# Kernel tuning notes

Hardware: AMD Instinct MI355X
Metric: run time of the kernel (lower is better)

The kernel has to match this reference:

```python
import jax, jax.numpy as jnp
import numpy as np
import math

D_MODEL = 1024
NUM_HEADS = 16
HEAD_DIM = D_MODEL // NUM_HEADS
WINDOW = 5  # positions j with i - W//2 <= j <= i + W//2 are visible


def setup_inputs() -> dict:
    key = jax.random.key(0)
    ks = jax.random.split(key, 9)
    B, S = 2, 2048
    x = jax.random.normal(ks[0], (B, S, D_MODEL), dtype=jnp.float32)
    # Xavier-uniform linear weights [out, in] (torch convention), zero biases
    lim = math.sqrt(6.0 / (D_MODEL + D_MODEL))
    def w(k):
        return jax.random.uniform(k, (D_MODEL, D_MODEL), dtype=jnp.float32, minval=-lim, maxval=lim)
    return {
        'x': x,
        'Wq': w(ks[1]), 'bq': jnp.zeros((D_MODEL,), jnp.float32),
        'Wk': w(ks[2]), 'bk': jnp.zeros((D_MODEL,), jnp.float32),
        'Wv': w(ks[3]), 'bv': jnp.zeros((D_MODEL,), jnp.float32),
        'Wo': w(ks[4]), 'bo': jnp.zeros((D_MODEL,), jnp.float32),
    }


def reference(x, Wq, bq, Wk, bk, Wv, bv, Wo, bo):
    B, S, D = x.shape
    H, hd = NUM_HEADS, HEAD_DIM
    half = WINDOW // 2

    def proj(W, b):
        # torch Linear: y = x @ W.T + b ; split heads -> [B, H, S, hd]
        return (jnp.einsum('bsd,ed->bse', x, W) + b).reshape(B, S, H, hd).transpose(0, 2, 1, 3)

    q = proj(Wq, bq)
    k = proj(Wk, bk)
    v = proj(Wv, bv)

    scores = jnp.einsum('bhqd,bhkd->bhqk', q, k) / jnp.sqrt(jnp.asarray(hd, x.dtype))
    i = jnp.arange(S)[:, None]
    j = jnp.arange(S)[None, :]
    band = (j >= i - half) & (j <= i + half)  # [S, S] local window mask
    scores = jnp.where(band, scores, jnp.asarray(-1e9, x.dtype))
    attn = jax.nn.softmax(scores, axis=-1)  # dropout is identity in eval mode
    out = jnp.einsum('bhqk,bhkd->bhqd', attn, v)
    out = out.transpose(0, 2, 1, 3).reshape(B, S, D)
    return jnp.einsum('bsd,ed->bse', out, Wo) + bo
```

## Files before the change

### kernel.cpp

```cpp
#include <hip/hip_runtime.h>
#include <hip/hip_bf16.h>

typedef __bf16 bf16_t;
typedef __bf16 bf16x4 __attribute__((ext_vector_type(4)));
typedef __bf16 bf16x8 __attribute__((ext_vector_type(8)));
typedef float f32x4 __attribute__((ext_vector_type(4)));

#define S_LEN 2048
#define DMODEL 1024
#define NHEADS 16
#define HDIM 64
#define BROWS 4096
#define QKVN 3072

__device__ __forceinline__ void async16(const void* g, void* l) {
  __builtin_amdgcn_global_load_lds(
      (const __attribute__((address_space(1))) void*)g,
      (__attribute__((address_space(3))) void*)l, 16, 0, 0);
}

__global__ __launch_bounds__(256) void cvt_all_kernel(
    const float* __restrict__ x, const float* __restrict__ Wq,
    const float* __restrict__ Wk, const float* __restrict__ Wv,
    const float* __restrict__ Wo, bf16_t* __restrict__ dst) {
  const int i = blockIdx.x * 256 + threadIdx.x;
  constexpr int XN4 = (BROWS * DMODEL) / 4;
  constexpr int WN4 = (DMODEL * DMODEL) / 4;
  const float* src;
  size_t off;
  if (i < XN4) {
    src = x;
    off = (size_t)i;
  } else {
    const int wi = i - XN4;
    const int w = wi >> 18;
    off = (size_t)(wi & (WN4 - 1));
    src = (w == 0) ? Wq : (w == 1) ? Wk : (w == 2) ? Wv : Wo;
  }
  const float4 v = *(const float4*)(src + off * 4);
  bf16x4 o;
  o[0] = (bf16_t)v.x;
  o[1] = (bf16_t)v.y;
  o[2] = (bf16_t)v.z;
  o[3] = (bf16_t)v.w;
  *(bf16x4*)(dst + (size_t)i * 4) = o;
}

#define BARR __builtin_amdgcn_s_barrier()
#define LGKM0 asm volatile("s_waitcnt lgkmcnt(0)" ::: "memory")
#define VMC3 asm volatile("s_waitcnt vmcnt(3)" ::: "memory")
#define VMC0 asm volatile("s_waitcnt vmcnt(0)" ::: "memory")

__global__ __launch_bounds__(512, 2) void gemm_qkv256_kernel(
    const bf16_t* __restrict__ A, const bf16_t* __restrict__ W,
    const float* __restrict__ bq, const float* __restrict__ bk,
    const float* __restrict__ bv, bf16_t* __restrict__ C) {
  constexpr int Kd = 1024;
  __shared__ char lds[114688];
  char* ldsA = lds;
  char* ldsB = lds + 65536;

  const int m0 = blockIdx.x * 256;
  const int n0 = blockIdx.y * 192;

  const int tid = threadIdx.x;
  const int lane = tid & 63;
  const int wid = tid >> 6;
  const int wr = wid >> 2;
  const int wc = wid & 3;
  const int fr = lane & 15;
  const int l16 = lane >> 4;

  f32x4 acc[8][3] = {};
  bf16x8 aA[4][2], bB[3][2];

  auto stageA = [&](int buf, int h, int kt) {
#pragma unroll
    for (int l = 0; l < 2; ++l) {
      const int idx = l * 512 + tid;
      const int r = idx >> 3;
      const int slot = idx & 7;
      async16((const char*)(A + (size_t)(m0 + h * 128 + r) * Kd + kt * 64 +
                            ((slot ^ (r & 7)) << 3)),
              ldsA + buf * 32768 + h * 16384 + r * 128 + slot * 16);
    }
  };
  auto stageB = [&](int buf, int th, int kt) {
    const int r = tid >> 3;
    const int slot = tid & 7;
    async16((const char*)(W + (size_t)(n0 + th * 64 + r) * Kd + kt * 64 +
                          ((slot ^ (r & 7)) << 3)),
            ldsB + buf * 24576 + th * 8192 + r * 128 + slot * 16);
  };

  auto rdA = [&](int buf, int row, int ks) -> bf16x8 {
    return *(const bf16x8*)(ldsA + buf * 32768 + row * 128 +
                            ((((ks << 2) + l16) ^ (row & 7)) << 4));
  };
  auto rdB = [&](int buf, int row, int ks) -> bf16x8 {
    return *(const bf16x8*)(ldsB + buf * 24576 + row * 128 +
                            ((((ks << 2) + l16) ^ (row & 7)) << 4));
  };

#define RDA(MH, BUF)                                                     \
  _Pragma("unroll") for (int m_ = 0; m_ < 4; ++m_)                       \
      _Pragma("unroll") for (int ks_ = 0; ks_ < 2; ++ks_) aA[m_][ks_] =  \
          rdA(BUF, wr * 128 + (MH)*64 + m_ * 16 + fr, ks_);
#define RDB(NF0, NC, BUF)                                                \
  _Pragma("unroll") for (int n_ = 0; n_ < (NC); ++n_)                    \
      _Pragma("unroll") for (int ks_ = 0; ks_ < 2; ++ks_)                \
          bB[(NF0) + n_][ks_] =                                          \
              rdB(BUF, wc * 48 + ((NF0) + n_) * 16 + fr, ks_);
#define MMAQ(MH, NF0, NC)                                                     \
  _Pragma("unroll") for (int m_ = 0; m_ < 4; ++m_)                            \
      _Pragma("unroll") for (int n_ = 0; n_ < (NC); ++n_) {                   \
    acc[(MH)*4 + m_][(NF0) + n_] = __builtin_amdgcn_mfma_f32_16x16x32_bf16(   \
        aA[m_][0], bB[(NF0) + n_][0], acc[(MH)*4 + m_][(NF0) + n_], 0, 0, 0); \
    acc[(MH)*4 + m_][(NF0) + n_] = __builtin_amdgcn_mfma_f32_16x16x32_bf16(   \
        aA[m_][1], bB[(NF0) + n_][1], acc[(MH)*4 + m_][(NF0) + n_], 0, 0, 0); \
  }

  stageA(0, 0, 0);
  stageA(0, 1, 0);
  stageB(0, 0, 0);
  stageB(0, 1, 0);
  stageB(0, 2, 0);
  stageB(1, 0, 1);
  stageB(1, 1, 1);
  stageB(1, 2, 1);
  VMC3;
  BARR;

#pragma unroll 1
  for (int i = 0; i < 8; ++i) {
    const int t0 = 2 * i, t1 = 2 * i + 1;
    const bool st = (i < 7);
    RDA(0, 0);
    RDB(0, 2, 0);
    stageA(1, 0, t1);
    BARR;
    LGKM0;
    __builtin_amdgcn_s_setprio(1);
    MMAQ(0, 0, 2);
    __builtin_amdgcn_s_setprio(0);
    BARR;
    RDB(2, 1, 0);
    stageA(1, 1, t1);
    BARR;
    LGKM0;
    __builtin_amdgcn_s_setprio(1);
    MMAQ(0, 2, 1);
    __builtin_amdgcn_s_setprio(0);
    BARR;
    RDA(1, 0);
    if (st) stageB(0, 0, t0 + 2);
    BARR;
    LGKM0;
    __builtin_amdgcn_s_setprio(1);
    MMAQ(1, 0, 2);
    __builtin_amdgcn_s_setprio(0);
    BARR;
    if (st) {
      stageB(0, 1, t0 + 2);
      stageB(0, 2, t0 + 2);
    }
    __builtin_amdgcn_s_setprio(1);
    MMAQ(1, 2, 1);
    __builtin_amdgcn_s_setprio(0);
    if (st) {
      VMC3;
    } else {
      VMC0;
    }
    BARR;
    RDA(0, 1);
    RDB(0, 2, 1);
    if (st) stageA(0, 0, t0 + 2);
    BARR;
    LGKM0;
    __builtin_amdgcn_s_setprio(1);
    MMAQ(0, 0, 2);
    __builtin_amdgcn_s_setprio(0);
    BARR;
    RDB(2, 1, 1);
    if (st) stageA(0, 1, t0 + 2);
    BARR;
    LGKM0;
    __builtin_amdgcn_s_setprio(1);
    MMAQ(0, 2, 1);
    __builtin_amdgcn_s_setprio(0);
    BARR;
    RDA(1, 1);
    if (st) stageB(1, 0, t1 + 2);
    BARR;
    LGKM0;
    __builtin_amdgcn_s_setprio(1);
    MMAQ(1, 0, 2);
    __builtin_amdgcn_s_setprio(0);
    BARR;
    if (st) {
      stageB(1, 1, t1 + 2);
      stageB(1, 2, t1 + 2);
    }
    __builtin_amdgcn_s_setprio(1);
    MMAQ(1, 2, 1);
    __builtin_amdgcn_s_setprio(0);
    if (st) VMC3;
    BARR;
  }
#undef RDA
#undef RDB
#undef MMAQ

  const int cr = l16 * 4;
#pragma unroll
  for (int nf = 0; nf < 3; ++nf) {
    const int col = n0 + wc * 48 + nf * 16 + fr;
    const int mat = col >> 10;
    const float* bp = (mat == 0) ? bq : (mat == 1) ? bk : bv;
    const float bval = bp[col & 1023];
#pragma unroll
    for (int mf = 0; mf < 8; ++mf) {
      const int row = m0 + wr * 128 + mf * 16 + cr;
#pragma unroll
      for (int r = 0; r < 4; ++r)
        C[(size_t)(row + r) * QKVN + col] = (bf16_t)(acc[mf][nf][r] + bval);
    }
  }
}

template <typename OutT>
__device__ __forceinline__ void gemm_body(
    const bf16_t* __restrict__ A, const bf16_t* __restrict__ W,
    const float* __restrict__ bias, OutT* __restrict__ C, int m0, int n0) {
  constexpr int Kd = 1024, Nd = 1024, BK = 32, NT = Kd / BK;
  __shared__ bf16_t ldsA[2][128 * BK];
  __shared__ bf16_t ldsB[2][128 * BK];

  const int tid = threadIdx.x;
  const int lane = tid & 63;
  const int wave = tid >> 6;
  const int wr = wave >> 1;
  const int wc = wave & 1;

  f32x4 acc[4][4] = {};

  const int fr = lane & 15;
  const int ko = (lane >> 4) * 8;

  auto stage = [&](int buf, int t) {
    const int k0 = t * BK;
#pragma unroll
    for (int p = 0; p < 2; ++p) {
      const int off = (p * 256 + tid) * 16;
      const int row = off >> 6;
      const int kb = off & 63;
      async16((const char*)(A + (size_t)(m0 + row) * Kd + k0) + kb,
              (char*)ldsA[buf] + off);
      async16((const char*)(W + (size_t)(n0 + row) * Kd + k0) + kb,
              (char*)ldsB[buf] + off);
    }
  };

  auto compute = [&](int buf) {
    bf16x8 af[4], bfr[4];
#pragma unroll
    for (int i = 0; i < 4; ++i)
      af[i] = *(const bf16x8*)(ldsA[buf] + (wr * 64 + i * 16 + fr) * BK + ko);
#pragma unroll
    for (int j = 0; j < 4; ++j)
      bfr[j] = *(const bf16x8*)(ldsB[buf] + (wc * 64 + j * 16 + fr) * BK + ko);
#pragma unroll
    for (int i = 0; i < 4; ++i)
#pragma unroll
      for (int j = 0; j < 4; ++j)
        acc[i][j] = __builtin_amdgcn_mfma_f32_16x16x32_bf16(af[i], bfr[j],
                                                            acc[i][j], 0, 0, 0);
  };

  stage(0, 0);
  __syncthreads();
#pragma unroll 1
  for (int t = 0; t < NT; ++t) {
    if (t + 1 < NT) stage((t + 1) & 1, t + 1);
    compute(t & 1);
    __syncthreads();
  }

  const int cr = (lane >> 4) * 4;
#pragma unroll
  for (int j = 0; j < 4; ++j) {
    const int col = n0 + wc * 64 + j * 16 + fr;
    const float bval = bias[col];
#pragma unroll
    for (int i = 0; i < 4; ++i) {
#pragma unroll
      for (int r = 0; r < 4; ++r) {
        const int row = m0 + wr * 64 + i * 16 + cr + r;
        C[(size_t)row * Nd + col] = (OutT)(acc[i][j][r] + bval);
      }
    }
  }
}

__global__ __launch_bounds__(256) void gemm_o_kernel(
    const bf16_t* __restrict__ ctx, const bf16_t* __restrict__ Wob,
    const float* __restrict__ bo, float* __restrict__ out) {
  gemm_body<float>(ctx, Wob, bo, out, blockIdx.x * 128, blockIdx.y * 128);
}

#define CHUNK 256
#define TROWS 260

__global__ __launch_bounds__(256) void attn_kernel(
    const bf16_t* __restrict__ QKV, bf16_t* __restrict__ ctx) {
  __shared__ bf16_t ldsK[TROWS * HDIM];
  __shared__ bf16_t ldsV[TROWS * HDIM];

  const int tid = threadIdx.x;
  const int blk = blockIdx.x;
  const int chunk = blk & 7;
  const int bh = blk >> 3;
  const int h = bh & (NHEADS - 1);
  const int b = bh >> 4;
  const int s0 = chunk * CHUNK;

  const bf16_t* Kb = QKV + (size_t)b * S_LEN * QKVN + DMODEL + h * HDIM;
  const bf16_t* Vb = QKV + (size_t)b * S_LEN * QKVN + 2 * DMODEL + h * HDIM;

#pragma unroll
  for (int j = 0; j < 9; ++j) {
    const int i = j * 256 + tid;
    if (i < TROWS * 8) {
      const int tr = i >> 3;
      const int slot = i & 7;
      const int c = slot ^ (tr & 7);
      int gs = s0 - 2 + tr;
      gs = (gs < 0) ? 0 : (gs >= S_LEN ? S_LEN - 1 : gs);
      async16((const char*)(Kb + (size_t)gs * QKVN) + c * 16,
              (char*)ldsK + i * 16);
      async16((const char*)(Vb + (size_t)gs * QKVN) + c * 16,
              (char*)ldsV + i * 16);
    }
  }

  const int s = s0 + tid;
  const bf16_t* Qrow = QKV + ((size_t)(b * S_LEN) + s) * QKVN + h * HDIM;
  bf16x8 q8[8];
#pragma unroll
  for (int c = 0; c < 8; ++c) q8[c] = *(const bf16x8*)(Qrow + c * 8);
  float qf[64];
#pragma unroll
  for (int c = 0; c < 8; ++c)
#pragma unroll
    for (int e = 0; e < 8; ++e) qf[c * 8 + e] = (float)q8[c][e];

  __syncthreads();

  float sc[5];
#pragma unroll
  for (int jj = 0; jj < 5; ++jj) {
    const int tr = tid + jj;
    float d = 0.f;
#pragma unroll
    for (int c = 0; c < 8; ++c) {
      const bf16x8 k8 = *(const bf16x8*)(ldsK + tr * HDIM + (c ^ (tr & 7)) * 8);
#pragma unroll
      for (int e = 0; e < 8; ++e) d += qf[c * 8 + e] * (float)k8[e];
    }
    const int j = s - 2 + jj;
    sc[jj] = (j < 0 || j >= S_LEN) ? -1e30f : d * 0.125f;
  }

  float m = sc[0];
#pragma unroll
  for (int jj = 1; jj < 5; ++jj) m = fmaxf(m, sc[jj]);
  float p[5], l = 0.f;
#pragma unroll
  for (int jj = 0; jj < 5; ++jj) {
    p[jj] = __expf(sc[jj] - m);
    l += p[jj];
  }
  const float inv = 1.0f / l;
#pragma unroll
  for (int jj = 0; jj < 5; ++jj) p[jj] *= inv;

  float o[64];
#pragma unroll
  for (int e = 0; e < 64; ++e) o[e] = 0.f;
#pragma unroll
  for (int jj = 0; jj < 5; ++jj) {
    const int tr = tid + jj;
    const float pj = p[jj];
#pragma unroll
    for (int c = 0; c < 8; ++c) {
      const bf16x8 v8 = *(const bf16x8*)(ldsV + tr * HDIM + (c ^ (tr & 7)) * 8);
#pragma unroll
      for (int e = 0; e < 8; ++e) o[c * 8 + e] += pj * (float)v8[e];
    }
  }

  bf16_t* Crow = (bf16_t*)ctx + ((size_t)(b * S_LEN) + s) * DMODEL + h * HDIM;
#pragma unroll
  for (int c = 0; c < 8; ++c) {
    bf16x8 ov;
#pragma unroll
    for (int e = 0; e < 8; ++e) ov[e] = (bf16_t)o[c * 8 + e];
    *(bf16x8*)(Crow + c * 8) = ov;
  }
}

extern "C" void kernel_launch(void* const* d_in, const int* in_sizes, int n_in,
                              void* d_out, int out_size, void* d_ws,
                              size_t ws_size, hipStream_t stream) {
  const float* x = (const float*)d_in[0];
  const float* Wq = (const float*)d_in[1];
  const float* bq = (const float*)d_in[2];
  const float* Wk = (const float*)d_in[3];
  const float* bk = (const float*)d_in[4];
  const float* Wv = (const float*)d_in[5];
  const float* bv = (const float*)d_in[6];
  const float* Wo = (const float*)d_in[7];
  const float* bo = (const float*)d_in[8];
  float* out = (float*)d_out;

  const size_t mat = (size_t)BROWS * DMODEL;
  const size_t wmat = (size_t)DMODEL * DMODEL;
  bf16_t* xb = (bf16_t*)d_ws;
  bf16_t* Wqkv = xb + mat;
  bf16_t* Wob = Wqkv + 3 * wmat;
  bf16_t* QKV = Wob + wmat;
  bf16_t* ctx = QKV + 3 * mat;

  cvt_all_kernel<<<8192, 256, 0, stream>>>(x, Wq, Wk, Wv, Wo, xb);

  gemm_qkv256_kernel<<<dim3(16, 16), 512, 0, stream>>>(xb, Wqkv, bq, bk, bv,
                                                       QKV);
  attn_kernel<<<256, 256, 0, stream>>>(QKV, ctx);
  gemm_o_kernel<<<dim3(32, 8), 256, 0, stream>>>(ctx, Wob, bo, out);
}
```

Measured before the change: 80.07 us.

## Double-buffer A fragments in registers and drop explicit LDS waits in QKV GEMM

The QKV GEMM main loop now keeps two register sets for A fragments. Both halves are read from LDS ahead of use, and the next k-tile's first half is prefetched before the closing barrier. The explicit lgkmcnt(0) waits are removed and replaced with sched_barrier fences, leaving the compiler to insert waits. The aim is to cut the number of LDS-read/barrier/MFMA phases and overlap LDS reads with MFMA work, at the cost of more VGPRs under a 512-thread, 2-block launch bound, which risks spills or lower occupancy.

```diff
diff --git a/kernel.cpp b/kernel.cpp
--- a/kernel.cpp
+++ b/kernel.cpp
@@ -47,7 +47,7 @@
 }
 
 #define BARR __builtin_amdgcn_s_barrier()
-#define LGKM0 asm volatile("s_waitcnt lgkmcnt(0)" ::: "memory")
+#define SB0 __builtin_amdgcn_sched_barrier(0)
 #define VMC3 asm volatile("s_waitcnt vmcnt(3)" ::: "memory")
 #define VMC0 asm volatile("s_waitcnt vmcnt(0)" ::: "memory")
 
@@ -72,7 +72,7 @@
   const int l16 = lane >> 4;
 
   f32x4 acc[8][3] = {};
-  bf16x8 aA[4][2], bB[3][2];
+  bf16x8 aS0[4][2], aS1[4][2], bB[3][2];
 
   auto stageA = [&](int buf, int h, int kt) {
 #pragma unroll
@@ -102,22 +102,22 @@
                             ((((ks << 2) + l16) ^ (row & 7)) << 4));
   };
 
-#define RDA(MH, BUF)                                                     \
+#define RDA_TO(AS, MH, BUF)                                              \
   _Pragma("unroll") for (int m_ = 0; m_ < 4; ++m_)                       \
-      _Pragma("unroll") for (int ks_ = 0; ks_ < 2; ++ks_) aA[m_][ks_] =  \
+      _Pragma("unroll") for (int ks_ = 0; ks_ < 2; ++ks_) AS[m_][ks_] =  \
           rdA(BUF, wr * 128 + (MH)*64 + m_ * 16 + fr, ks_);
 #define RDB(NF0, NC, BUF)                                                \
   _Pragma("unroll") for (int n_ = 0; n_ < (NC); ++n_)                    \
       _Pragma("unroll") for (int ks_ = 0; ks_ < 2; ++ks_)                \
           bB[(NF0) + n_][ks_] =                                          \
               rdB(BUF, wc * 48 + ((NF0) + n_) * 16 + fr, ks_);
-#define MMAQ(MH, NF0, NC)                                                     \
+#define MMAQ(AS, MH, NF0, NC)                                                 \
   _Pragma("unroll") for (int m_ = 0; m_ < 4; ++m_)                            \
       _Pragma("unroll") for (int n_ = 0; n_ < (NC); ++n_) {                   \
     acc[(MH)*4 + m_][(NF0) + n_] = __builtin_amdgcn_mfma_f32_16x16x32_bf16(   \
-        aA[m_][0], bB[(NF0) + n_][0], acc[(MH)*4 + m_][(NF0) + n_], 0, 0, 0); \
+        AS[m_][0], bB[(NF0) + n_][0], acc[(MH)*4 + m_][(NF0) + n_], 0, 0, 0); \
     acc[(MH)*4 + m_][(NF0) + n_] = __builtin_amdgcn_mfma_f32_16x16x32_bf16(   \
-        aA[m_][1], bB[(NF0) + n_][1], acc[(MH)*4 + m_][(NF0) + n_], 0, 0, 0); \
+        AS[m_][1], bB[(NF0) + n_][1], acc[(MH)*4 + m_][(NF0) + n_], 0, 0, 0); \
   }
 
   stageA(0, 0, 0);
@@ -130,85 +130,94 @@
   stageB(1, 2, 1);
   VMC3;
   BARR;
+  RDA_TO(aS0, 0, 0);
 
 #pragma unroll 1
   for (int i = 0; i < 8; ++i) {
     const int t0 = 2 * i, t1 = 2 * i + 1;
     const bool st = (i < 7);
-    RDA(0, 0);
     RDB(0, 2, 0);
+    RDA_TO(aS1, 1, 0);
     stageA(1, 0, t1);
-    BARR;
-    LGKM0;
-    __builtin_amdgcn_s_setprio(1);
-    MMAQ(0, 0, 2);
+    SB0;
+    BARR;
+    __builtin_amdgcn_s_setprio(1);
+    MMAQ(aS0, 0, 0, 2);
     __builtin_amdgcn_s_setprio(0);
     BARR;
     RDB(2, 1, 0);
     stageA(1, 1, t1);
-    BARR;
-    LGKM0;
-    __builtin_amdgcn_s_setprio(1);
-    MMAQ(0, 2, 1);
-    __builtin_amdgcn_s_setprio(0);
-    BARR;
-    RDA(1, 0);
+    SB0;
+    BARR;
+    __builtin_amdgcn_s_setprio(1);
+    MMAQ(aS0, 0, 2, 1);
+    __builtin_amdgcn_s_setprio(0);
+    BARR;
     if (st) stageB(0, 0, t0 + 2);
-    BARR;
-    LGKM0;
-    __builtin_amdgcn_s_setprio(1);
-    MMAQ(1, 0, 2);
+    SB0;
+    BARR;
+    __builtin_amdgcn_s_setprio(1);
+    MMAQ(aS1, 1, 0, 2);
     __builtin_amdgcn_s_setprio(0);
     BARR;
     if (st) {
       stageB(0, 1, t0 + 2);
       stageB(0, 2, t0 + 2);
     }
-    __builtin_amdgcn_s_setprio(1);
-    MMAQ(1, 2, 1);
-    __builtin_amdgcn_s_setprio(0);
+    SB0;
+    __builtin_amdgcn_s_setprio(1);
+    MMAQ(aS1, 1, 2, 1);
+    __builtin_amdgcn_s_setprio(0);
+    SB0;
     if (st) {
       VMC3;
     } else {
       VMC0;
     }
-    BARR;
-    RDA(0, 1);
+    RDA_TO(aS0, 0, 1);
+    SB0;
+    BARR;
     RDB(0, 2, 1);
+    RDA_TO(aS1, 1, 1);
     if (st) stageA(0, 0, t0 + 2);
-    BARR;
-    LGKM0;
-    __builtin_amdgcn_s_setprio(1);
-    MMAQ(0, 0, 2);
+    SB0;
+    BARR;
+    __builtin_amdgcn_s_setprio(1);
+    MMAQ(aS0, 0, 0, 2);
     __builtin_amdgcn_s_setprio(0);
     BARR;
     RDB(2, 1, 1);
     if (st) stageA(0, 1, t0 + 2);
-    BARR;
-    LGKM0;
-    __builtin_amdgcn_s_setprio(1);
-    MMAQ(0, 2, 1);
-    __builtin_amdgcn_s_setprio(0);
-    BARR;
-    RDA(1, 1);
+    SB0;
+    BARR;
+    __builtin_amdgcn_s_setprio(1);
+    MMAQ(aS0, 0, 2, 1);
+    __builtin_amdgcn_s_setprio(0);
+    BARR;
     if (st) stageB(1, 0, t1 + 2);
-    BARR;
-    LGKM0;
-    __builtin_amdgcn_s_setprio(1);
-    MMAQ(1, 0, 2);
+    SB0;
+    BARR;
+    __builtin_amdgcn_s_setprio(1);
+    MMAQ(aS1, 1, 0, 2);
     __builtin_amdgcn_s_setprio(0);
     BARR;
     if (st) {
       stageB(1, 1, t1 + 2);
       stageB(1, 2, t1 + 2);
     }
-    __builtin_amdgcn_s_setprio(1);
-    MMAQ(1, 2, 1);
-    __builtin_amdgcn_s_setprio(0);
-    if (st) VMC3;
-    BARR;
-  }
-#undef RDA
+    SB0;
+    __builtin_amdgcn_s_setprio(1);
+    MMAQ(aS1, 1, 2, 1);
+    __builtin_amdgcn_s_setprio(0);
+    SB0;
+    if (st) {
+      VMC3;
+      RDA_TO(aS0, 0, 0);
+    }
+    SB0;
+    BARR;
+  }
+#undef RDA_TO
 #undef RDB
 #undef MMAQ
 
```

After: 77.92 us. -2.7%, faster.
